# Optimization experiments

Measured on AMD Instinct MI355X. Metric: run time of the kernel, lower is better.

Reference implementation:

```python
import jax, jax.numpy as jnp
import numpy as np

N, F = 1024, 512
H, W = 128, 128
TANX = TANY = 0.5
SCALE_MOD = 1.0


def quat_to_rot(q):
    q = q / jnp.linalg.norm(q, axis=-1, keepdims=True)
    r, x, y, z = q[:, 0], q[:, 1], q[:, 2], q[:, 3]
    R = jnp.stack([
        1 - 2 * (y * y + z * z), 2 * (x * y - r * z), 2 * (x * z + r * y),
        2 * (x * y + r * z), 1 - 2 * (x * x + z * z), 2 * (y * z - r * x),
        2 * (x * z - r * y), 2 * (y * z + r * x), 1 - 2 * (x * x + y * y)], -1)
    return R.reshape(-1, 3, 3)


def setup_inputs() -> dict:
    key = jax.random.key(0)
    ks = jax.random.split(key, 9)
    u = jax.random.uniform(ks[0], (N, 3))
    # place gaussians in front of the camera (z in [2,6], x/y within frustum)
    means3D = jnp.stack([(u[:, 0] - 0.5) * 2.0, (u[:, 1] - 0.5) * 2.0,
                         2.0 + 4.0 * u[:, 2]], axis=1)
    means2D = jnp.zeros((N, 3), jnp.float32)  # grad holder, unused in fwd math
    opacities = 0.05 + 0.9 * jax.random.uniform(ks[1], (N, 1))
    colors_precomp = jax.random.uniform(ks[2], (N, 3))
    semantic_feature = jax.random.uniform(ks[3], (N, F))
    scales = 0.02 + 0.08 * jax.random.uniform(ks[4], (N, 3))
    rotations = jax.random.normal(ks[5], (N, 4))
    viewmatrix = jnp.eye(4, dtype=jnp.float32)
    znear, zfar = 0.01, 100.0
    P = np.zeros((4, 4), np.float32)
    P[0, 0] = 1.0 / TANX
    P[1, 1] = 1.0 / TANY
    P[2, 2] = zfar / (zfar - znear)
    P[2, 3] = -zfar * znear / (zfar - znear)
    P[3, 2] = 1.0
    projmatrix = jnp.asarray(P.T)  # row-vector convention p_h @ M (3DGS style)
    bg = jnp.zeros(3, jnp.float32)
    campos = jnp.zeros(3, jnp.float32)
    conv_w = 0.02 * jax.random.normal(ks[6], (512, F))
    conv_b = 0.01 * jax.random.normal(ks[7], (512,))
    return dict(means3D=means3D, means2D=means2D, opacities=opacities,
                colors_precomp=colors_precomp, semantic_feature=semantic_feature,
                scales=scales, rotations=rotations, viewmatrix=viewmatrix,
                projmatrix=projmatrix, bg=bg, campos=campos,
                conv_w=conv_w, conv_b=conv_b)


def _rasterize(means3D, opacities, colors_precomp, semantic_feature, scales,
               rotations, viewmatrix, projmatrix, bg):
    n = means3D.shape[0]
    ph = jnp.concatenate([means3D, jnp.ones((n, 1), means3D.dtype)], 1)
    p_view = ph @ viewmatrix                     # [N,4] camera space
    p_hom = ph @ projmatrix                      # [N,4] clip space
    p_proj = p_hom[:, :3] / (p_hom[:, 3:4] + 1e-7)
    depth = p_view[:, 2]

    # 3D covariance: Sigma = R S S^T R^T
    R = quat_to_rot(rotations)
    M = R * (scales * SCALE_MOD)[:, None, :]
    cov3D = M @ jnp.swapaxes(M, 1, 2)            # [N,3,3]

    # EWA projection to 2D covariance
    fx, fy = W / (2 * TANX), H / (2 * TANY)
    tz = p_view[:, 2]
    txz = jnp.clip(p_view[:, 0] / tz, -1.3 * TANX, 1.3 * TANX) * tz
    tyz = jnp.clip(p_view[:, 1] / tz, -1.3 * TANY, 1.3 * TANY) * tz
    J = jnp.zeros((n, 2, 3), means3D.dtype)
    J = J.at[:, 0, 0].set(fx / tz).at[:, 0, 2].set(-fx * txz / (tz * tz))
    J = J.at[:, 1, 1].set(fy / tz).at[:, 1, 2].set(-fy * tyz / (tz * tz))
    T = J @ viewmatrix[:3, :3].T[None]           # [N,2,3]
    cov2D = T @ cov3D @ jnp.swapaxes(T, 1, 2)
    cov2D = cov2D.at[:, 0, 0].add(0.3).at[:, 1, 1].add(0.3)  # low-pass dilation

    det = cov2D[:, 0, 0] * cov2D[:, 1, 1] - cov2D[:, 0, 1] ** 2
    det_safe = jnp.where(det == 0, 1.0, det)
    conic = jnp.stack([cov2D[:, 1, 1], -cov2D[:, 0, 1], cov2D[:, 0, 0]], -1) / det_safe[:, None]

    mid = 0.5 * (cov2D[:, 0, 0] + cov2D[:, 1, 1])
    lam1 = mid + jnp.sqrt(jnp.maximum(0.1, mid * mid - det))
    radii = jnp.ceil(3.0 * jnp.sqrt(lam1)).astype(jnp.int32)

    px = ((p_proj[:, 0] + 1.0) * W - 1.0) * 0.5  # ndc2Pix
    py = ((p_proj[:, 1] + 1.0) * H - 1.0) * 0.5
    valid = (depth > 0.2) & (det != 0)
    radii = jnp.where(valid, radii, 0)

    order = jnp.argsort(depth)                   # global front-to-back sort
    gy, gx = jnp.meshgrid(jnp.arange(H, dtype=means3D.dtype),
                          jnp.arange(W, dtype=means3D.dtype), indexing='ij')
    dx = px[order][:, None, None] - gx[None]     # [N,H,W]
    dy = py[order][:, None, None] - gy[None]
    co = conic[order]
    power = (-0.5 * (co[:, 0, None, None] * dx * dx
                     + co[:, 2, None, None] * dy * dy)
             - co[:, 1, None, None] * dx * dy)
    alpha = jnp.minimum(0.99, opacities[order][:, 0, None, None] * jnp.exp(power))
    keep = (power <= 0) & (alpha >= 1.0 / 255.0) & valid[order][:, None, None]
    alpha = jnp.where(keep, alpha, 0.0)

    log1m = jnp.log1p(-alpha)                    # log transmittance increments
    Texcl = jnp.exp(jnp.cumsum(log1m, axis=0) - log1m)  # exclusive cumprod
    w = Texcl * alpha                            # [N,H,W] blend weights
    Tfinal = jnp.exp(jnp.sum(log1m, axis=0))     # [H,W]

    color = jnp.einsum('nhw,nc->chw', w, colors_precomp[order]) \
        + Tfinal[None] * bg[:, None, None]
    feature_map = jnp.einsum('nhw,nf->fhw', w, semantic_feature[order])
    return color, feature_map, radii


def reference(means3D, means2D, opacities, colors_precomp, semantic_feature,
              scales, rotations, viewmatrix, projmatrix, bg, campos,
              conv_w, conv_b):
    color, feature_map, radii = _rasterize(
        means3D, opacities, colors_precomp, semantic_feature, scales,
        rotations, viewmatrix, projmatrix, bg)
    # final 1x1 conv on the rendered feature map
    feature_out = jnp.einsum('fhw,of->ohw', feature_map, conv_w) \
        + conv_b[:, None, None]
    return color, feature_out, radii
```

## Files before the change

### kernel.cpp

```cpp
#include <hip/hip_runtime.h>
#include <hip/hip_bf16.h>
#include <math.h>

#define H_IMG 128
#define W_IMG 128
#define N_G   1024
#define F_DIM 512
#define O_DIM 512
#define PIX   (H_IMG*W_IMG)
#define FEAT_OFF 49152
#define RAD_OFF  (49152 + 512*16384)
#define MAXG  192
#define WT_PITCH 200
#define GT_PITCH 72

typedef __attribute__((ext_vector_type(8))) short bf16x8;
typedef __attribute__((ext_vector_type(4))) float f32x4;

__global__ __launch_bounds__(256) void preprank_kernel(
    const float* __restrict__ means,
    const float* __restrict__ opac,
    const float* __restrict__ colors,
    const float* __restrict__ scales,
    const float* __restrict__ rots,
    const float* __restrict__ view,
    const float* __restrict__ proj,
    int* __restrict__ order,
    float* __restrict__ psort,
    float* __restrict__ csort,
    float* __restrict__ rb,
    float* __restrict__ radii_out)
{
    __shared__ float d[N_G];
    __shared__ int pr[64][4];
    const int t = threadIdx.x;
    const float v2 = view[2], v6 = view[6], v10 = view[10], v14 = view[14];
    for (int i = t; i < N_G; i += 256)
        d[i] = means[3*i]*v2 + means[3*i+1]*v6 + means[3*i+2]*v10 + v14;
    __syncthreads();

    const int ln = t & 63;
    const int ch = t >> 6;
    const int n  = blockIdx.x*64 + ln;
    const float depth = d[n];

    {
        int rp = 0;
        const int mbeg = ch*256;
        for (int m = mbeg; m < mbeg + 256; ++m) {
            float dm = d[m];
            rp += (dm < depth) || (dm == depth && m < n);
        }
        pr[ln][ch] = rp;
    }
    __syncthreads();
    if (ch != 0) return;

    const int r = pr[ln][0] + pr[ln][1] + pr[ln][2] + pr[ln][3];

    float x = means[3*n], y = means[3*n+1], z = means[3*n+2];
    float pv0 = x*view[0] + y*view[4] + z*view[8]  + view[12];
    float pv1 = x*view[1] + y*view[5] + z*view[9]  + view[13];
    float ph0 = x*proj[0] + y*proj[4] + z*proj[8]  + proj[12];
    float ph1 = x*proj[1] + y*proj[5] + z*proj[9]  + proj[13];
    float phw = x*proj[3] + y*proj[7] + z*proj[11] + proj[15];
    float denom = phw + 1e-7f;
    float pp0 = ph0/denom, pp1 = ph1/denom;

    float qr=rots[4*n], qx=rots[4*n+1], qy=rots[4*n+2], qz=rots[4*n+3];
    float qn = sqrtf(qr*qr+qx*qx+qy*qy+qz*qz);
    qr/=qn; qx/=qn; qy/=qn; qz/=qn;
    float R00=1.f-2.f*(qy*qy+qz*qz), R01=2.f*(qx*qy-qr*qz), R02=2.f*(qx*qz+qr*qy);
    float R10=2.f*(qx*qy+qr*qz), R11=1.f-2.f*(qx*qx+qz*qz), R12=2.f*(qy*qz-qr*qx);
    float R20=2.f*(qx*qz-qr*qy), R21=2.f*(qy*qz+qr*qx), R22=1.f-2.f*(qx*qx+qy*qy);
    float s0=scales[3*n], s1=scales[3*n+1], s2=scales[3*n+2];
    float M00=R00*s0, M01=R01*s1, M02=R02*s2;
    float M10=R10*s0, M11=R11*s1, M12=R12*s2;
    float M20=R20*s0, M21=R21*s1, M22=R22*s2;
    float c00=M00*M00+M01*M01+M02*M02;
    float c01=M00*M10+M01*M11+M02*M12;
    float c02=M00*M20+M01*M21+M02*M22;
    float c11=M10*M10+M11*M11+M12*M12;
    float c12=M10*M20+M11*M21+M12*M22;
    float c22=M20*M20+M21*M21+M22*M22;

    const float fx=128.f, fy=128.f;
    float tz = depth;
    float txz = fminf(fmaxf(pv0/tz, -0.65f), 0.65f) * tz;
    float tyz = fminf(fmaxf(pv1/tz, -0.65f), 0.65f) * tz;
    float J00 = fx/tz,  J02 = -fx*txz/(tz*tz);
    float J11 = fy/tz,  J12 = -fy*tyz/(tz*tz);
    float T00=J00*view[0] + J02*view[2];
    float T01=J00*view[4] + J02*view[6];
    float T02=J00*view[8] + J02*view[10];
    float T10=J11*view[1] + J12*view[2];
    float T11=J11*view[5] + J12*view[6];
    float T12=J11*view[9] + J12*view[10];
    float u0 = T00*c00 + T01*c01 + T02*c02;
    float u1 = T00*c01 + T01*c11 + T02*c12;
    float u2 = T00*c02 + T01*c12 + T02*c22;
    float v0 = T10*c00 + T11*c01 + T12*c02;
    float v1 = T10*c01 + T11*c11 + T12*c12;
    float v2r= T10*c02 + T11*c12 + T12*c22;
    float a00 = u0*T00 + u1*T01 + u2*T02 + 0.3f;
    float a01 = u0*T10 + u1*T11 + u2*T12;
    float a11 = v0*T10 + v1*T11 + v2r*T12 + 0.3f;

    float det = a00*a11 - a01*a01;
    float dsafe = (det==0.f) ? 1.f : det;
    float inv = 1.f/dsafe;
    float con0 =  a11*inv, con1 = -a01*inv, con2 = a00*inv;
    float mid = 0.5f*(a00+a11);
    float lam1 = mid + sqrtf(fmaxf(0.1f, mid*mid - det));
    int irad = (int)ceilf(3.f*sqrtf(lam1));
    float pxc = ((pp0+1.f)*128.f - 1.f)*0.5f;
    float pyc = ((pp1+1.f)*128.f - 1.f)*0.5f;
    bool valid = (depth > 0.2f) && (det != 0.f);

    radii_out[n] = valid ? (float)irad : 0.f;
    order[r] = n;
    float* p = psort + 8*r;
    p[0]=pxc; p[1]=pyc; p[2]=con0; p[3]=con1; p[4]=con2;
    p[5]=opac[n]; p[6]=depth; p[7]= valid ? 1.f : 0.f;
    csort[4*r+0] = colors[3*n+0];
    csort[4*r+1] = colors[3*n+1];
    csort[4*r+2] = colors[3*n+2];
    csort[4*r+3] = 0.f;

    float op = opac[n];
    float tau = logf(255.f * op);
    bool active = valid && (tau > 0.f);
    float rx = active ? (sqrtf(2.f*tau*a00) + 0.01f) : -1.f;
    float ry = active ? (sqrtf(2.f*tau*a11) + 0.01f) : -1.f;
    rb[2*r+0] = rx;
    rb[2*r+1] = ry;
}

__global__ __launch_bounds__(256) void gemmG_kernel(const float* __restrict__ S,
                                                    const float* __restrict__ Wm,
                                                    const int* __restrict__ order,
                                                    __hip_bfloat16* __restrict__ Gvb)
{
    const int t    = threadIdx.x;
    const int lane = t & 63;
    const int wv   = t >> 6;
    const int m0   = blockIdx.y * 64 + wv * 16;
    const int o0   = blockIdx.x * 16;
    const int lhi  = lane >> 4;
    const int llo  = lane & 15;

    const int arow = order[m0 + llo] & (N_G - 1);
    const float* Ar = S  + (size_t)arow*F_DIM + 8*lhi;
    const float* Br = Wm + (size_t)(o0 + llo)*F_DIM + 8*lhi;

    f32x4 acc = (f32x4){0.f,0.f,0.f,0.f};

    float4 a0 = *reinterpret_cast<const float4*>(Ar);
    float4 a1 = *reinterpret_cast<const float4*>(Ar + 4);
    float4 b0 = *reinterpret_cast<const float4*>(Br);
    float4 b1 = *reinterpret_cast<const float4*>(Br + 4);

    for (int k0 = 0; k0 < F_DIM; k0 += 32) {
        float4 na0, na1, nb0, nb1;
        const bool more = (k0 + 32) < F_DIM;
        if (more) {
            na0 = *reinterpret_cast<const float4*>(Ar + k0 + 32);
            na1 = *reinterpret_cast<const float4*>(Ar + k0 + 36);
            nb0 = *reinterpret_cast<const float4*>(Br + k0 + 32);
            nb1 = *reinterpret_cast<const float4*>(Br + k0 + 36);
        }
        bf16x8 af, bf;
        af[0]=__bfloat16_as_short(__float2bfloat16(a0.x));
        af[1]=__bfloat16_as_short(__float2bfloat16(a0.y));
        af[2]=__bfloat16_as_short(__float2bfloat16(a0.z));
        af[3]=__bfloat16_as_short(__float2bfloat16(a0.w));
        af[4]=__bfloat16_as_short(__float2bfloat16(a1.x));
        af[5]=__bfloat16_as_short(__float2bfloat16(a1.y));
        af[6]=__bfloat16_as_short(__float2bfloat16(a1.z));
        af[7]=__bfloat16_as_short(__float2bfloat16(a1.w));
        bf[0]=__bfloat16_as_short(__float2bfloat16(b0.x));
        bf[1]=__bfloat16_as_short(__float2bfloat16(b0.y));
        bf[2]=__bfloat16_as_short(__float2bfloat16(b0.z));
        bf[3]=__bfloat16_as_short(__float2bfloat16(b0.w));
        bf[4]=__bfloat16_as_short(__float2bfloat16(b1.x));
        bf[5]=__bfloat16_as_short(__float2bfloat16(b1.y));
        bf[6]=__bfloat16_as_short(__float2bfloat16(b1.z));
        bf[7]=__bfloat16_as_short(__float2bfloat16(b1.w));
        acc = __builtin_amdgcn_mfma_f32_16x16x32_bf16(af, bf, acc, 0, 0, 0);
        if (more) { a0 = na0; a1 = na1; b0 = nb0; b1 = nb1; }
    }

    #pragma unroll
    for (int r = 0; r < 4; ++r) {
        int row = m0 + 4*lhi + r;
        Gvb[(size_t)row*O_DIM + o0 + llo] = __float2bfloat16(acc[r]);
    }
}

__global__ __launch_bounds__(1024) void alphafeat_kernel(
    const float* __restrict__ psort, const float* __restrict__ csort,
    const float* __restrict__ rb, const float* __restrict__ bg,
    const __hip_bfloat16* __restrict__ Gvb, const float* __restrict__ conv_b,
    float* __restrict__ out)
{
    __shared__ __align__(16) char uni[73728];
    float (*pg)[8]       = (float(*)[8])uni;
    float (*cs)[4]       = (float(*)[4])(uni + 32768);
    float (*colbuf)[64][4] = (float(*)[64][4])(uni + 49152);
    float (*Pl)[64]      = (float(*)[64])(uni + 65536);
    short (*GT)[GT_PITCH] = (short(*)[GT_PITCH])uni;

    __shared__ short WT[64][WT_PITCH];
    __shared__ float rbl[N_G][2];
    __shared__ float Tfl[64];
    __shared__ int   idx_lds[MAXG];
    __shared__ int   cntl_s[16];
    __shared__ int   cnt_tot;

    const int t    = threadIdx.x;
    const int c    = t >> 6;
    const int lane = t & 63;
    const int tile = blockIdx.x;
    const int hrow = tile >> 1;
    const int w0   = (tile & 1) * 64;

    {
        float4* pgv = reinterpret_cast<float4*>(&pg[0][0]);
        const float4* ps4 = reinterpret_cast<const float4*>(psort);
        pgv[t]        = ps4[t];
        pgv[t + 1024] = ps4[t + 1024];
        float4* csv = reinterpret_cast<float4*>(&cs[0][0]);
        csv[t] = reinterpret_cast<const float4*>(csort)[t];
        reinterpret_cast<float2*>(&rbl[0][0])[t] =
            reinterpret_cast<const float2*>(rb)[t];
        int* wtz = (int*)&WT[0][0];
        for (int i = t; i < 64*WT_PITCH/2; i += 1024) wtz[i] = 0;
        if (t < MAXG) idx_lds[t] = 0;
    }
    __syncthreads();

    const float gx = (float)(w0 + lane);
    const float gy = (float)hrow;
    const float wlo = (float)w0;
    const float whi = (float)(w0 + 63);

    unsigned long long hitmask;
    {
        int g = c*64 + lane;
        float2 R = *reinterpret_cast<const float2*>(&rbl[g][0]);
        float2 Axy = *reinterpret_cast<const float2*>(&pg[g][0]);
        bool hit = (R.x >= 0.f) && (fabsf(Axy.y - gy) <= R.y)
                && (Axy.x >= wlo - R.x) && (Axy.x <= whi + R.x);
        hitmask = __ballot(hit);
    }

    float pref = 1.f;
    int cnt = 0;
    {
        unsigned long long m = hitmask;
        while (m) {
            int j = (int)__builtin_ctzll(m); m &= m - 1;
            int g = c*64 + j;
            float4 A = *reinterpret_cast<const float4*>(&pg[g][0]);
            float4 B = *reinterpret_cast<const float4*>(&pg[g][4]);
            float dx = A.x - gx, dy = A.y - gy;
            float pw = -0.5f*(A.z*dx*dx + B.x*dy*dy) - A.w*dx*dy;
            float al = fminf(0.99f, B.y*__expf(pw));
            bool keep = (pw <= 0.f) && (al >= (1.f/255.f)) && (B.w > 0.5f);
            float a = keep ? al : 0.f;
            float w = pref * a;
            pref *= 1.f - a;
            cnt += (__ballot(w > 1e-12f) != 0ull) ? 1 : 0;
        }
    }
    Pl[c][lane] = pref;
    if (lane == 0) cntl_s[c] = cnt;
    __syncthreads();

    int base = 0;
    float cp = 1.f;
    for (int cc = 0; cc < c; ++cc) {
        base += cntl_s[cc];
        cp *= Pl[cc][lane];
    }
    if (c == 15) {
        Tfl[lane] = cp * Pl[15][lane];
        if (lane == 0) {
            int tot = base + cntl_s[15];
            cnt_tot = (tot < MAXG) ? tot : MAXG;
        }
    }

    float pref2 = 1.f;
    int slot = base;
    float col0 = 0.f, col1 = 0.f, col2 = 0.f;
    {
        unsigned long long m = hitmask;
        while (m) {
            int j = (int)__builtin_ctzll(m); m &= m - 1;
            int g = c*64 + j;
            float4 A = *reinterpret_cast<const float4*>(&pg[g][0]);
            float4 B = *reinterpret_cast<const float4*>(&pg[g][4]);
            float dx = A.x - gx, dy = A.y - gy;
            float pw = -0.5f*(A.z*dx*dx + B.x*dy*dy) - A.w*dx*dy;
            float al = fminf(0.99f, B.y*__expf(pw));
            bool keep = (pw <= 0.f) && (al >= (1.f/255.f)) && (B.w > 0.5f);
            float a = keep ? al : 0.f;
            float w = pref2 * a;
            pref2 *= 1.f - a;
            if (__ballot(w > 1e-12f) != 0ull) {
                float wfin = w * cp;
                if (slot < MAXG) {
                    WT[lane][slot] = __bfloat16_as_short(__float2bfloat16(wfin));
                    if (lane == 0) idx_lds[slot] = g;
                }
                float4 cv = *reinterpret_cast<const float4*>(&cs[g][0]);
                col0 += wfin*cv.x; col1 += wfin*cv.y; col2 += wfin*cv.z;
                ++slot;
            }
        }
    }

    colbuf[c][lane][0] = col0; colbuf[c][lane][1] = col1; colbuf[c][lane][2] = col2;
    __syncthreads();

    if (t < 64) {
        float r = 0.f, g = 0.f, b = 0.f;
        #pragma unroll
        for (int k = 0; k < 16; ++k) {
            r += colbuf[k][t][0]; g += colbuf[k][t][1]; b += colbuf[k][t][2];
        }
        float Tf = Tfl[t];
        int pix = hrow*W_IMG + w0 + t;
        out[0*PIX + pix] = r + Tf*bg[0];
        out[1*PIX + pix] = g + Tf*bg[1];
        out[2*PIX + pix] = b + Tf*bg[2];
    }
    __syncthreads();

    int scnt = cnt_tot;
    scnt = (scnt < 0) ? 0 : ((scnt > MAXG) ? MAXG : scnt);
    const short* gvs = (const short*)Gvb;

    f32x4 acc[2][4];
    #pragma unroll
    for (int i = 0; i < 2; ++i)
        #pragma unroll
        for (int j = 0; j < 4; ++j)
            acc[i][j] = (f32x4){0.f,0.f,0.f,0.f};

    const int nchunk = (scnt + 63) >> 6;
    for (int cc = 0; cc < nchunk; ++cc) {
        const int kbase = cc*64;
        {
            const int o = t & 511;
            const int half = t >> 9;
            #pragma unroll
            for (int b = 0; b < 4; ++b) {
                bf16x8 s;
                #pragma unroll
                for (int j = 0; j < 8; ++j) {
                    int k = kbase + half*32 + b*8 + j;
                    s[j] = (k < scnt) ? gvs[(size_t)idx_lds[k]*O_DIM + o] : (short)0;
                }
                *(bf16x8*)&GT[o][half*32 + b*8] = s;
            }
        }
        __syncthreads();

        #pragma unroll
        for (int ks = 0; ks < 2; ++ks) {
            const int kf = 8*(lane>>4);
            bf16x8 bfr[4];
            #pragma unroll
            for (int pt = 0; pt < 4; ++pt)
                bfr[pt] = *(const bf16x8*)&WT[pt*16 + (lane&15)][kbase + ks*32 + kf];
            #pragma unroll
            for (int ot = 0; ot < 2; ++ot) {
                bf16x8 af = *(const bf16x8*)&GT[c*32 + ot*16 + (lane&15)][ks*32 + kf];
                #pragma unroll
                for (int pt = 0; pt < 4; ++pt)
                    acc[ot][pt] = __builtin_amdgcn_mfma_f32_16x16x32_bf16(
                        af, bfr[pt], acc[ot][pt], 0, 0, 0);
            }
        }
        __syncthreads();
    }

    const int pixbase = hrow*W_IMG + w0;
    #pragma unroll
    for (int ot = 0; ot < 2; ++ot) {
        #pragma unroll
        for (int r = 0; r < 4; ++r) {
            int o = c*32 + ot*16 + 4*(lane>>4) + r;
            float cb = conv_b[o];
            #pragma unroll
            for (int pt = 0; pt < 4; ++pt) {
                out[FEAT_OFF + (size_t)o*PIX + pixbase + pt*16 + (lane&15)]
                    = acc[ot][pt][r] + cb;
            }
        }
    }
}

extern "C" void kernel_launch(void* const* d_in, const int* in_sizes, int n_in,
                              void* d_out, int out_size, void* d_ws, size_t ws_size,
                              hipStream_t stream)
{
    const float* means  = (const float*)d_in[0];
    const float* opac   = (const float*)d_in[2];
    const float* colors = (const float*)d_in[3];
    const float* sem    = (const float*)d_in[4];
    const float* scales = (const float*)d_in[5];
    const float* rots   = (const float*)d_in[6];
    const float* view   = (const float*)d_in[7];
    const float* proj   = (const float*)d_in[8];
    const float* bg     = (const float*)d_in[9];
    const float* conv_w = (const float*)d_in[11];
    const float* conv_b = (const float*)d_in[12];
    float* out = (float*)d_out;

    float* wsf   = (float*)d_ws;
    float* psort = wsf;
    float* csort = wsf + 8192;
    int*   order = (int*)(wsf + 12288);
    float* rb    = wsf + 13312;
    __hip_bfloat16* Gvb = (__hip_bfloat16*)(wsf + 16384);

    float* radii_out = out + RAD_OFF;

    preprank_kernel<<<16, 256, 0, stream>>>(means, opac, colors, scales, rots,
                                            view, proj, order, psort, csort,
                                            rb, radii_out);
    gemmG_kernel<<<dim3(32,16), 256, 0, stream>>>(sem, conv_w, order, Gvb);
    alphafeat_kernel<<<256, 1024, 0, stream>>>(psort, csort, rb, bg, Gvb,
                                               conv_b, out);
}
```

Baseline: 54.34 us.

## Shrink LDS footprint and split output channels into two passes

Colour and radius/bbox arrays are no longer staged in shared memory; they are read directly from global memory. The union buffer shrinks and colbuf drops its padding lane. The feature GEMM now runs in two halves of 256 output channels, so the GT staging tile and accumulator count are halved. This lowers LDS and register use, which may let more blocks fit per CU. The cost is repeating the chunk loop and the WT fragment reads per half, plus scattered global reads for colours.

```diff
diff --git a/kernel.cpp b/kernel.cpp
--- a/kernel.cpp
+++ b/kernel.cpp
@@ -203,15 +203,13 @@
     const __hip_bfloat16* __restrict__ Gvb, const float* __restrict__ conv_b,
     float* __restrict__ out)
 {
-    __shared__ __align__(16) char uni[73728];
-    float (*pg)[8]       = (float(*)[8])uni;
-    float (*cs)[4]       = (float(*)[4])(uni + 32768);
-    float (*colbuf)[64][4] = (float(*)[64][4])(uni + 49152);
-    float (*Pl)[64]      = (float(*)[64])(uni + 65536);
+    __shared__ __align__(16) char uni[49152];
+    float (*pg)[8]        = (float(*)[8])uni;
+    float (*colbuf)[64][3]= (float(*)[64][3])(uni + 32768);
+    float (*Pl)[64]       = (float(*)[64])(uni + 45056);
     short (*GT)[GT_PITCH] = (short(*)[GT_PITCH])uni;
 
     __shared__ short WT[64][WT_PITCH];
-    __shared__ float rbl[N_G][2];
     __shared__ float Tfl[64];
     __shared__ int   idx_lds[MAXG];
     __shared__ int   cntl_s[16];
@@ -229,10 +227,6 @@
         const float4* ps4 = reinterpret_cast<const float4*>(psort);
         pgv[t]        = ps4[t];
         pgv[t + 1024] = ps4[t + 1024];
-        float4* csv = reinterpret_cast<float4*>(&cs[0][0]);
-        csv[t] = reinterpret_cast<const float4*>(csort)[t];
-        reinterpret_cast<float2*>(&rbl[0][0])[t] =
-            reinterpret_cast<const float2*>(rb)[t];
         int* wtz = (int*)&WT[0][0];
         for (int i = t; i < 64*WT_PITCH/2; i += 1024) wtz[i] = 0;
         if (t < MAXG) idx_lds[t] = 0;
@@ -247,7 +241,7 @@
     unsigned long long hitmask;
     {
         int g = c*64 + lane;
-        float2 R = *reinterpret_cast<const float2*>(&rbl[g][0]);
+        float2 R = reinterpret_cast<const float2*>(rb)[g];
         float2 Axy = *reinterpret_cast<const float2*>(&pg[g][0]);
         bool hit = (R.x >= 0.f) && (fabsf(Axy.y - gy) <= R.y)
                 && (Axy.x >= wlo - R.x) && (Axy.x <= whi + R.x);
@@ -314,7 +308,7 @@
                     WT[lane][slot] = __bfloat16_as_short(__float2bfloat16(wfin));
                     if (lane == 0) idx_lds[slot] = g;
                 }
-                float4 cv = *reinterpret_cast<const float4*>(&cs[g][0]);
+                float4 cv = *reinterpret_cast<const float4*>(&csort[4*g]);
                 col0 += wfin*cv.x; col1 += wfin*cv.y; col2 += wfin*cv.z;
                 ++slot;
             }
@@ -341,63 +335,57 @@
     int scnt = cnt_tot;
     scnt = (scnt < 0) ? 0 : ((scnt > MAXG) ? MAXG : scnt);
     const short* gvs = (const short*)Gvb;
-
-    f32x4 acc[2][4];
-    #pragma unroll
-    for (int i = 0; i < 2; ++i)
+    const int nchunk = (scnt + 63) >> 6;
+    const int pixbase = hrow*W_IMG + w0;
+
+    for (int h = 0; h < 2; ++h) {
+        const int ob = h * 256;
+        f32x4 acc[4];
         #pragma unroll
-        for (int j = 0; j < 4; ++j)
-            acc[i][j] = (f32x4){0.f,0.f,0.f,0.f};
-
-    const int nchunk = (scnt + 63) >> 6;
-    for (int cc = 0; cc < nchunk; ++cc) {
-        const int kbase = cc*64;
-        {
-            const int o = t & 511;
-            const int half = t >> 9;
+        for (int j = 0; j < 4; ++j) acc[j] = (f32x4){0.f,0.f,0.f,0.f};
+
+        for (int cc = 0; cc < nchunk; ++cc) {
+            const int kbase = cc*64;
+            {
+                const int ol = t & 255;
+                const int kg = t >> 8;
+                #pragma unroll
+                for (int b = 0; b < 2; ++b) {
+                    bf16x8 s;
+                    #pragma unroll
+                    for (int j = 0; j < 8; ++j) {
+                        int k = kbase + kg*16 + b*8 + j;
+                        s[j] = (k < scnt) ? gvs[(size_t)idx_lds[k]*O_DIM + ob + ol] : (short)0;
+                    }
+                    *(bf16x8*)&GT[ol][kg*16 + b*8] = s;
+                }
+            }
+            __syncthreads();
+
             #pragma unroll
-            for (int b = 0; b < 4; ++b) {
-                bf16x8 s;
-                #pragma unroll
-                for (int j = 0; j < 8; ++j) {
-                    int k = kbase + half*32 + b*8 + j;
-                    s[j] = (k < scnt) ? gvs[(size_t)idx_lds[k]*O_DIM + o] : (short)0;
-                }
-                *(bf16x8*)&GT[o][half*32 + b*8] = s;
-            }
-        }
-        __syncthreads();
-
-        #pragma unroll
-        for (int ks = 0; ks < 2; ++ks) {
-            const int kf = 8*(lane>>4);
-            bf16x8 bfr[4];
-            #pragma unroll
-            for (int pt = 0; pt < 4; ++pt)
-                bfr[pt] = *(const bf16x8*)&WT[pt*16 + (lane&15)][kbase + ks*32 + kf];
-            #pragma unroll
-            for (int ot = 0; ot < 2; ++ot) {
-                bf16x8 af = *(const bf16x8*)&GT[c*32 + ot*16 + (lane&15)][ks*32 + kf];
+            for (int ks = 0; ks < 2; ++ks) {
+                const int kf = 8*(lane>>4);
+                bf16x8 bfr[4];
                 #pragma unroll
                 for (int pt = 0; pt < 4; ++pt)
-                    acc[ot][pt] = __builtin_amdgcn_mfma_f32_16x16x32_bf16(
-                        af, bfr[pt], acc[ot][pt], 0, 0, 0);
+                    bfr[pt] = *(const bf16x8*)&WT[pt*16 + (lane&15)][kbase + ks*32 + kf];
+                bf16x8 af = *(const bf16x8*)&GT[c*16 + (lane&15)][ks*32 + kf];
+                #pragma unroll
+                for (int pt = 0; pt < 4; ++pt)
+                    acc[pt] = __builtin_amdgcn_mfma_f32_16x16x32_bf16(
+                        af, bfr[pt], acc[pt], 0, 0, 0);
             }
-        }
-        __syncthreads();
-    }
-
-    const int pixbase = hrow*W_IMG + w0;
-    #pragma unroll
-    for (int ot = 0; ot < 2; ++ot) {
+            __syncthreads();
+        }
+
         #pragma unroll
         for (int r = 0; r < 4; ++r) {
-            int o = c*32 + ot*16 + 4*(lane>>4) + r;
+            int o = ob + c*16 + 4*(lane>>4) + r;
             float cb = conv_b[o];
             #pragma unroll
             for (int pt = 0; pt < 4; ++pt) {
                 out[FEAT_OFF + (size_t)o*PIX + pixbase + pt*16 + (lane&15)]
-                    = acc[ot][pt][r] + cb;
+                    = acc[pt][r] + cb;
             }
         }
     }
```

New measurement: 57.46 us. +5.7%, slower.

## Merge preprocessing and feature GEMM into one launch by dropping sorted-row gather

Applied to the files above, without the earlier changes.

The 1x1-conv GEMM no longer depends on the depth ranking. It projects the semantic features in their original Gaussian order, so it can run in the same launch as the preprocessing and ranking blocks (blocks 16 and up do the GEMM). Each sorted record now stores its original Gaussian index in the slot that held depth, and the blend kernel uses that index to pick the projected feature row. This removes one kernel launch, the order buffer and the dependency between the two stages. In exchange, the depth value is no longer kept in the sorted record and a float-to-int index conversion is added.

```diff
diff --git a/kernel.cpp b/kernel.cpp
--- a/kernel.cpp
+++ b/kernel.cpp
@@ -17,7 +17,7 @@
 typedef __attribute__((ext_vector_type(8))) short bf16x8;
 typedef __attribute__((ext_vector_type(4))) float f32x4;
 
-__global__ __launch_bounds__(256) void preprank_kernel(
+__global__ __launch_bounds__(256) void prep_gemm_kernel(
     const float* __restrict__ means,
     const float* __restrict__ opac,
     const float* __restrict__ colors,
@@ -25,12 +25,74 @@
     const float* __restrict__ rots,
     const float* __restrict__ view,
     const float* __restrict__ proj,
-    int* __restrict__ order,
+    const float* __restrict__ S,
+    const float* __restrict__ Wm,
     float* __restrict__ psort,
     float* __restrict__ csort,
     float* __restrict__ rb,
-    float* __restrict__ radii_out)
+    float* __restrict__ radii_out,
+    __hip_bfloat16* __restrict__ Gvb)
 {
+    const int bid = blockIdx.x;
+    if (bid >= 16) {
+        const int id   = bid - 16;
+        const int t    = threadIdx.x;
+        const int lane = t & 63;
+        const int wv   = t >> 6;
+        const int m0   = (id >> 5) * 64 + wv * 16;
+        const int o0   = (id & 31) * 16;
+        const int lhi  = lane >> 4;
+        const int llo  = lane & 15;
+
+        const int arow = m0 + llo;
+        const float* Ar = S  + (size_t)arow*F_DIM + 8*lhi;
+        const float* Br = Wm + (size_t)(o0 + llo)*F_DIM + 8*lhi;
+
+        f32x4 acc = (f32x4){0.f,0.f,0.f,0.f};
+
+        float4 a0 = *reinterpret_cast<const float4*>(Ar);
+        float4 a1 = *reinterpret_cast<const float4*>(Ar + 4);
+        float4 b0 = *reinterpret_cast<const float4*>(Br);
+        float4 b1 = *reinterpret_cast<const float4*>(Br + 4);
+
+        for (int k0 = 0; k0 < F_DIM; k0 += 32) {
+            float4 na0, na1, nb0, nb1;
+            const bool more = (k0 + 32) < F_DIM;
+            if (more) {
+                na0 = *reinterpret_cast<const float4*>(Ar + k0 + 32);
+                na1 = *reinterpret_cast<const float4*>(Ar + k0 + 36);
+                nb0 = *reinterpret_cast<const float4*>(Br + k0 + 32);
+                nb1 = *reinterpret_cast<const float4*>(Br + k0 + 36);
+            }
+            bf16x8 af, bf;
+            af[0]=__bfloat16_as_short(__float2bfloat16(a0.x));
+            af[1]=__bfloat16_as_short(__float2bfloat16(a0.y));
+            af[2]=__bfloat16_as_short(__float2bfloat16(a0.z));
+            af[3]=__bfloat16_as_short(__float2bfloat16(a0.w));
+            af[4]=__bfloat16_as_short(__float2bfloat16(a1.x));
+            af[5]=__bfloat16_as_short(__float2bfloat16(a1.y));
+            af[6]=__bfloat16_as_short(__float2bfloat16(a1.z));
+            af[7]=__bfloat16_as_short(__float2bfloat16(a1.w));
+            bf[0]=__bfloat16_as_short(__float2bfloat16(b0.x));
+            bf[1]=__bfloat16_as_short(__float2bfloat16(b0.y));
+            bf[2]=__bfloat16_as_short(__float2bfloat16(b0.z));
+            bf[3]=__bfloat16_as_short(__float2bfloat16(b0.w));
+            bf[4]=__bfloat16_as_short(__float2bfloat16(b1.x));
+            bf[5]=__bfloat16_as_short(__float2bfloat16(b1.y));
+            bf[6]=__bfloat16_as_short(__float2bfloat16(b1.z));
+            bf[7]=__bfloat16_as_short(__float2bfloat16(b1.w));
+            acc = __builtin_amdgcn_mfma_f32_16x16x32_bf16(af, bf, acc, 0, 0, 0);
+            if (more) { a0 = na0; a1 = na1; b0 = nb0; b1 = nb1; }
+        }
+
+        #pragma unroll
+        for (int r = 0; r < 4; ++r) {
+            int row = m0 + 4*lhi + r;
+            Gvb[(size_t)row*O_DIM + o0 + llo] = __float2bfloat16(acc[r]);
+        }
+        return;
+    }
+
     __shared__ float d[N_G];
     __shared__ int pr[64][4];
     const int t = threadIdx.x;
@@ -41,7 +103,7 @@
 
     const int ln = t & 63;
     const int ch = t >> 6;
-    const int n  = blockIdx.x*64 + ln;
+    const int n  = bid*64 + ln;
     const float depth = d[n];
 
     {
@@ -118,10 +180,9 @@
     bool valid = (depth > 0.2f) && (det != 0.f);
 
     radii_out[n] = valid ? (float)irad : 0.f;
-    order[r] = n;
     float* p = psort + 8*r;
     p[0]=pxc; p[1]=pyc; p[2]=con0; p[3]=con1; p[4]=con2;
-    p[5]=opac[n]; p[6]=depth; p[7]= valid ? 1.f : 0.f;
+    p[5]=opac[n]; p[6]=(float)n; p[7]= valid ? 1.f : 0.f;
     csort[4*r+0] = colors[3*n+0];
     csort[4*r+1] = colors[3*n+1];
     csort[4*r+2] = colors[3*n+2];
@@ -134,67 +195,6 @@
     float ry = active ? (sqrtf(2.f*tau*a11) + 0.01f) : -1.f;
     rb[2*r+0] = rx;
     rb[2*r+1] = ry;
-}
-
-__global__ __launch_bounds__(256) void gemmG_kernel(const float* __restrict__ S,
-                                                    const float* __restrict__ Wm,
-                                                    const int* __restrict__ order,
-                                                    __hip_bfloat16* __restrict__ Gvb)
-{
-    const int t    = threadIdx.x;
-    const int lane = t & 63;
-    const int wv   = t >> 6;
-    const int m0   = blockIdx.y * 64 + wv * 16;
-    const int o0   = blockIdx.x * 16;
-    const int lhi  = lane >> 4;
-    const int llo  = lane & 15;
-
-    const int arow = order[m0 + llo] & (N_G - 1);
-    const float* Ar = S  + (size_t)arow*F_DIM + 8*lhi;
-    const float* Br = Wm + (size_t)(o0 + llo)*F_DIM + 8*lhi;
-
-    f32x4 acc = (f32x4){0.f,0.f,0.f,0.f};
-
-    float4 a0 = *reinterpret_cast<const float4*>(Ar);
-    float4 a1 = *reinterpret_cast<const float4*>(Ar + 4);
-    float4 b0 = *reinterpret_cast<const float4*>(Br);
-    float4 b1 = *reinterpret_cast<const float4*>(Br + 4);
-
-    for (int k0 = 0; k0 < F_DIM; k0 += 32) {
-        float4 na0, na1, nb0, nb1;
-        const bool more = (k0 + 32) < F_DIM;
-        if (more) {
-            na0 = *reinterpret_cast<const float4*>(Ar + k0 + 32);
-            na1 = *reinterpret_cast<const float4*>(Ar + k0 + 36);
-            nb0 = *reinterpret_cast<const float4*>(Br + k0 + 32);
-            nb1 = *reinterpret_cast<const float4*>(Br + k0 + 36);
-        }
-        bf16x8 af, bf;
-        af[0]=__bfloat16_as_short(__float2bfloat16(a0.x));
-        af[1]=__bfloat16_as_short(__float2bfloat16(a0.y));
-        af[2]=__bfloat16_as_short(__float2bfloat16(a0.z));
-        af[3]=__bfloat16_as_short(__float2bfloat16(a0.w));
-        af[4]=__bfloat16_as_short(__float2bfloat16(a1.x));
-        af[5]=__bfloat16_as_short(__float2bfloat16(a1.y));
-        af[6]=__bfloat16_as_short(__float2bfloat16(a1.z));
-        af[7]=__bfloat16_as_short(__float2bfloat16(a1.w));
-        bf[0]=__bfloat16_as_short(__float2bfloat16(b0.x));
-        bf[1]=__bfloat16_as_short(__float2bfloat16(b0.y));
-        bf[2]=__bfloat16_as_short(__float2bfloat16(b0.z));
-        bf[3]=__bfloat16_as_short(__float2bfloat16(b0.w));
-        bf[4]=__bfloat16_as_short(__float2bfloat16(b1.x));
-        bf[5]=__bfloat16_as_short(__float2bfloat16(b1.y));
-        bf[6]=__bfloat16_as_short(__float2bfloat16(b1.z));
-        bf[7]=__bfloat16_as_short(__float2bfloat16(b1.w));
-        acc = __builtin_amdgcn_mfma_f32_16x16x32_bf16(af, bf, acc, 0, 0, 0);
-        if (more) { a0 = na0; a1 = na1; b0 = nb0; b1 = nb1; }
-    }
-
-    #pragma unroll
-    for (int r = 0; r < 4; ++r) {
-        int row = m0 + 4*lhi + r;
-        Gvb[(size_t)row*O_DIM + o0 + llo] = __float2bfloat16(acc[r]);
-    }
 }
 
 __global__ __launch_bounds__(1024) void alphafeat_kernel(
@@ -312,7 +312,7 @@
                 float wfin = w * cp;
                 if (slot < MAXG) {
                     WT[lane][slot] = __bfloat16_as_short(__float2bfloat16(wfin));
-                    if (lane == 0) idx_lds[slot] = g;
+                    if (lane == 0) idx_lds[slot] = (int)B.z;
                 }
                 float4 cv = *reinterpret_cast<const float4*>(&cs[g][0]);
                 col0 += wfin*cv.x; col1 += wfin*cv.y; col2 += wfin*cv.z;
@@ -423,16 +423,14 @@
     float* wsf   = (float*)d_ws;
     float* psort = wsf;
     float* csort = wsf + 8192;
-    int*   order = (int*)(wsf + 12288);
     float* rb    = wsf + 13312;
     __hip_bfloat16* Gvb = (__hip_bfloat16*)(wsf + 16384);
 
     float* radii_out = out + RAD_OFF;
 
-    preprank_kernel<<<16, 256, 0, stream>>>(means, opac, colors, scales, rots,
-                                            view, proj, order, psort, csort,
-                                            rb, radii_out);
-    gemmG_kernel<<<dim3(32,16), 256, 0, stream>>>(sem, conv_w, order, Gvb);
+    prep_gemm_kernel<<<528, 256, 0, stream>>>(means, opac, colors, scales,
+                                              rots, view, proj, sem, conv_w,
+                                              psort, csort, rb, radii_out, Gvb);
     alphafeat_kernel<<<256, 1024, 0, stream>>>(psort, csort, rb, bg, Gvb,
                                                conv_b, out);
 }
```

Result: faster. 43.85 us (-19.3%).
